# Kernel optimization log

Measured on AMD Instinct MI355X. Metric: run time of the kernel, lower is better.

Reference implementation:

```python
import jax, jax.numpy as jnp
import numpy as np

V, H, COND_DIM, WIDTH = 256, 256, 64, 64
K_STEPS = 5
T = 1.0
GAMMA_W_MAX = 0.05
NOISE_FRAC = 0.1


def setup_inputs() -> dict:
    key = jax.random.key(0)
    ks = jax.random.split(key, 8)
    B = 32768
    # binary visible data (0/1 floats)
    v_data = (jax.random.uniform(ks[0], (B, V)) < 0.5).astype(jnp.float32)
    cond = jax.random.normal(ks[1], (B, COND_DIM), dtype=jnp.float32)
    W = 0.1 * jax.random.normal(ks[2], (V, H), dtype=jnp.float32)
    b = jnp.zeros((V,), jnp.float32)
    c = jnp.zeros((H,), jnp.float32)
    fc1_w = jax.random.normal(ks[3], (WIDTH, COND_DIM), dtype=jnp.float32) * (1.0 / np.sqrt(COND_DIM))
    fc1_b = jnp.zeros((WIDTH,), jnp.float32)
    # fc2 is zero-init in the original; use small random values so the
    # conditional scale/shift path is numerically exercised.
    fc2_w = 0.01 * jax.random.normal(ks[4], (2 * V + 4 * H, WIDTH), dtype=jnp.float32)
    fc2_b = jnp.zeros((2 * V + 4 * H,), jnp.float32)
    return {"v_data": v_data, "cond": cond, "W": W, "b": b, "c": c,
            "fc1_w": fc1_w, "fc1_b": fc1_b, "fc2_w": fc2_w, "fc2_b": fc2_b}


def _cond_params(cond, b, c, fc1_w, fc1_b, fc2_w, fc2_b):
    x = jnp.tanh(cond @ fc1_w.T + fc1_b)
    y = x @ fc2_w.T + fc2_b
    gb, bb, gc, bc, gw, _bw = jnp.split(y, np.cumsum([V, V, H, H, H])[:5].tolist(), axis=-1)
    b_mod = (1.0 + gb) * b[None, :] + bb            # [B,V]
    c_mod = (1.0 + gc) * c[None, :] + bc            # [B,H]
    w_scale = 1.0 + GAMMA_W_MAX * jnp.tanh(gw)      # [B,H]  (beta_w_max=0 -> no shift)
    return b_mod, c_mod, w_scale


def _free_energy_sym(v, W, b_mod, c_mod, w_scale):
    vW = (v @ W) * w_scale                          # [B,H]
    Wsum = W.sum(axis=0)[None, :] * w_scale         # [B,H]
    lin_v = vW + c_mod
    lin_f = Wsum - vW + c_mod
    t2v = jax.nn.softplus(lin_v).sum(axis=-1)
    t2f = jax.nn.softplus(lin_f).sum(axis=-1)
    t1v = -(v * b_mod).sum(axis=-1)
    t1f = -((1.0 - v) * b_mod).sum(axis=-1)
    fe_v = t1v - t2v
    fe_f = t1f - t2f
    stacked = jnp.stack([-fe_v, -fe_f], axis=-1)
    return -T * jax.nn.logsumexp(stacked / T, axis=-1)


def reference(v_data, cond, W, b, c, fc1_w, fc1_b, fc2_w, fc2_b):
    b_mod, c_mod, w_scale = _cond_params(cond, b, c, fc1_w, fc1_b, fc2_w, fc2_b)

    rng = jax.random.key(42)
    B = v_data.shape[0]
    n_noise = int(B * NOISE_FRAC)
    rng, kn = jax.random.split(rng)
    noise = (jax.random.uniform(kn, (n_noise, V)) < 0.5).astype(v_data.dtype)
    v_model = v_data.at[:n_noise].set(noise)

    def gibbs_step(carry, _):
        v, key = carry
        key, k1, k2 = jax.random.split(key, 3)
        p_h = jax.nn.sigmoid(((v @ W) * w_scale + c_mod) / T)
        h = (jax.random.uniform(k1, p_h.shape) < p_h).astype(v.dtype)
        p_v = jax.nn.sigmoid(((h * w_scale) @ W.T + b_mod) / T)
        v_new = (jax.random.uniform(k2, p_v.shape) < p_v).astype(v.dtype)
        return (v_new, key), None

    (v_model, _), _ = jax.lax.scan(gibbs_step, (v_model, rng), None, length=K_STEPS)
    v_model = jax.lax.stop_gradient(v_model)

    fe_data = _free_energy_sym(v_data, W, b_mod, c_mod, w_scale)
    fe_model = _free_energy_sym(v_model, W, b_mod, c_mod, w_scale)
    return (fe_data - fe_model).mean()
```

## Files before the change

kernel.cpp:

```cpp
#include <hip/hip_runtime.h>
#include <stdint.h>

#define V 256
#define H 256
#define CONDD 64
#define WIDTH 64
#define KSTEPS 5
#define BR 32
#define GWMAX 0.05f
#define SW(r) (((r) & 15) << 4)
#define SWX(r) (((r) & 7) << 4)

typedef __attribute__((ext_vector_type(8))) short s16x8;
typedef __attribute__((ext_vector_type(4))) short s16x4;
typedef __attribute__((ext_vector_type(4))) float f32x4;

__device__ __forceinline__ uint64_t splitmix64(uint64_t x) {
  x += 0x9E3779B97F4A7C15ULL;
  x = (x ^ (x >> 30)) * 0xBF58476D1CE4E5B9ULL;
  x = (x ^ (x >> 27)) * 0x94D049BB133111EBULL;
  return x ^ (x >> 31);
}
__device__ __forceinline__ unsigned short f2bf(float f) {
  uint32_t u = __float_as_uint(f);
  return (unsigned short)((u + 0x7FFFu + ((u >> 16) & 1u)) >> 16);
}
__device__ __forceinline__ float bf2f(unsigned short s) {
  return __uint_as_float(((uint32_t)s) << 16);
}
__device__ __forceinline__ uint32_t pack2(float lo, float hi) {
  return (uint32_t)f2bf(lo) | ((uint32_t)f2bf(hi) << 16);
}
__device__ __forceinline__ float unpk_lo(uint32_t u) { return bf2f((unsigned short)(u & 0xFFFFu)); }
__device__ __forceinline__ float unpk_hi(uint32_t u) { return bf2f((unsigned short)(u >> 16)); }
__device__ __forceinline__ float lcg_u01(uint64_t& s) {
  s = s * 6364136223846793005ULL + 1442695040888963407ULL;
  return (float)(uint32_t)(s >> 40) * (1.0f / 16777216.0f);
}
__device__ __forceinline__ float softplusf(float x) {
  return fmaxf(x, 0.0f) + log1pf(expf(-fabsf(x)));
}

__global__ void k_prep(const float* __restrict__ W, const float* __restrict__ fc2_w,
                       unsigned short* __restrict__ Wp_hi, unsigned short* __restrict__ Wp_lo,
                       unsigned short* __restrict__ WTp_hi, unsigned short* __restrict__ fc2p,
                       float* __restrict__ Wsum, float* __restrict__ out) {
  int bid = blockIdx.x;
  if (bid < 256) {
    int idx = bid * 256 + threadIdx.x;
    int j = idx & 7, l = (idx >> 3) & 63, nt = (idx >> 9) & 15, ks = idx >> 13;
    int kk = ks * 32 + (l >> 4) * 8 + j;
    int n = nt * 16 + (l & 15);
    float wv = W[(size_t)kk * H + n];
    unsigned short hi = f2bf(wv);
    Wp_hi[idx] = hi;
    Wp_lo[idx] = f2bf(wv - bf2f(hi));
    WTp_hi[idx] = f2bf(W[(size_t)n * H + kk]);
  } else if (bid < 576) {
    int idx = (bid - 256) * 256 + threadIdx.x;
    int j = idx & 7, l = (idx >> 3) & 63;
    int f = idx >> 9;
    int ks = f / 80, nt = f % 80;
    fc2p[idx] = f2bf(fc2_w[(size_t)(nt * 16 + (l & 15)) * WIDTH + ks * 32 + (l >> 4) * 8 + j]);
  } else {
    int h = threadIdx.x;
    float s = 0.f;
    for (int v = 0; v < V; ++v) s += W[(size_t)v * H + h];
    Wsum[h] = s;
    if (h == 0) out[0] = 0.0f;
  }
}

__device__ __forceinline__ void mm_pass(const char* srcL, const unsigned short* __restrict__ Wp,
                                        int w, int lc, int lg, f32x4 acc[2][2]) {
#pragma unroll
  for (int ks = 0; ks < 8; ++ks) {
    s16x8 af[2];
#pragma unroll
    for (int rt = 0; rt < 2; ++rt) {
      int r = rt * 16 + lc;
      af[rt] = *(const s16x8*)(srcL + r * 512 + ((ks * 64 + lg * 16) ^ SW(r)));
    }
#pragma unroll
    for (int n = 0; n < 2; ++n) {
      int f = ks * 16 + 2 * w + n;
      s16x8 bf = *(const s16x8*)(Wp + ((size_t)f * 64 + lg * 16 + lc) * 8);
#pragma unroll
      for (int rt = 0; rt < 2; ++rt)
        acc[rt][n] = __builtin_amdgcn_mfma_f32_16x16x32_bf16(af[rt], bf, acc[rt][n], 0, 0, 0);
    }
  }
}

__device__ __forceinline__ void fc2_slice(const s16x8 afx[2][2],
                                          const unsigned short* __restrict__ fc2p,
                                          int w, int l, int slice, f32x4 acc[2][2]) {
#pragma unroll
  for (int rt = 0; rt < 2; ++rt)
#pragma unroll
    for (int n = 0; n < 2; ++n) acc[rt][n] = (f32x4){0.f, 0.f, 0.f, 0.f};
#pragma unroll
  for (int ks = 0; ks < 2; ++ks)
#pragma unroll
    for (int n = 0; n < 2; ++n) {
      int f = ks * 80 + slice * 16 + 2 * w + n;
      s16x8 bf = *(const s16x8*)(fc2p + ((size_t)f * 64 + l) * 8);
#pragma unroll
      for (int rt = 0; rt < 2; ++rt)
        acc[rt][n] = __builtin_amdgcn_mfma_f32_16x16x32_bf16(afx[ks][rt], bf, acc[rt][n], 0, 0, 0);
    }
}

__global__ __launch_bounds__(512) void rbm_mfma(
    const float* __restrict__ v_data, const float* __restrict__ cond,
    const float* __restrict__ bvec, const float* __restrict__ cvec,
    const float* __restrict__ fc1_w, const float* __restrict__ fc1_b,
    const float* __restrict__ fc2_b, const unsigned short* __restrict__ Wp_hi,
    const unsigned short* __restrict__ Wp_lo, const unsigned short* __restrict__ WTp_hi,
    const unsigned short* __restrict__ fc2p, const float* __restrict__ Wsum,
    float* __restrict__ out, int Btot, int nnoise) {
  const int tid = threadIdx.x;
  const int w = tid >> 6, l = tid & 63, lc = l & 15, lg = l >> 4;
  const int row0 = blockIdx.x * BR;

  __shared__ unsigned short vmL[BR * 256];
  __shared__ unsigned short hwL[BR * 256];
  __shared__ float red[BR][8];

  uint64_t rs = splitmix64(((uint64_t)(blockIdx.x * 512 + tid) << 1) | 1ULL);

  if (tid < BR * 8) ((float*)red)[tid] = 0.0f;

  float* condS = (float*)hwL;
  char* xS = (char*)hwL + BR * 68 * 4;

#pragma unroll
  for (int s = 0; s < 4; ++s) {
    int e = s * 512 + tid, r = e >> 6, k = e & 63;
    condS[r * 68 + k] = cond[(size_t)(row0 + r) * CONDD + k];
  }
#pragma unroll
  for (int s = 0; s < 2; ++s) {
    int unit = s * 512 + tid;
    int r = unit >> 5, c0 = (unit & 31) * 8;
    int g = row0 + r;
    s16x8 pk;
    if (g < nnoise) {
      rs = rs * 6364136223846793005ULL + 1442695040888963407ULL;
      uint32_t bits = (uint32_t)(rs >> 32);
#pragma unroll
      for (int j = 0; j < 8; ++j) pk[j] = (short)(((bits >> j) & 1u) ? 0x3F80 : 0);
    } else {
      const float* src = v_data + (size_t)g * 256 + c0;
      float4 a = *(const float4*)src, b = *(const float4*)(src + 4);
      pk[0] = (short)f2bf(a.x); pk[1] = (short)f2bf(a.y);
      pk[2] = (short)f2bf(a.z); pk[3] = (short)f2bf(a.w);
      pk[4] = (short)f2bf(b.x); pk[5] = (short)f2bf(b.y);
      pk[6] = (short)f2bf(b.z); pk[7] = (short)f2bf(b.w);
    }
    *(s16x8*)((char*)vmL + r * 512 + ((c0 * 2) ^ SW(r))) = pk;
  }
  __syncthreads();

  {
    int r = tid >> 4, j0 = (tid & 15) * 4;
    float a4[4];
#pragma unroll
    for (int j = 0; j < 4; ++j) a4[j] = fc1_b[j0 + j];
    for (int k = 0; k < CONDD; ++k) {
      float cv = condS[r * 68 + k];
#pragma unroll
      for (int j = 0; j < 4; ++j)
        a4[j] = fmaf(cv, fc1_w[(size_t)(j0 + j) * CONDD + k], a4[j]);
    }
    s16x4 xp;
#pragma unroll
    for (int j = 0; j < 4; ++j) xp[j] = (short)f2bf(tanhf(a4[j]));
    *(s16x4*)(xS + r * 128 + ((j0 * 2) ^ SWX(r))) = xp;
  }
  __syncthreads();

  uint32_t cmws[2][2][4];
  uint32_t bmp[2][4];
  {
    s16x8 afx[2][2];
#pragma unroll
    for (int ks = 0; ks < 2; ++ks)
#pragma unroll
      for (int rt = 0; rt < 2; ++rt) {
        int r = rt * 16 + lc;
        afx[ks][rt] = *(const s16x8*)(xS + r * 128 + (((ks * 32 + lg * 8) * 2) ^ SWX(r)));
      }
    f32x4 accA[2][2], accB[2][2];
    fc2_slice(afx, fc2p, w, l, 0, accA);
    fc2_slice(afx, fc2p, w, l, 1, accB);
#pragma unroll
    for (int rt = 0; rt < 2; ++rt)
#pragma unroll
      for (int i = 0; i < 4; ++i) {
        float b0, b1;
        {
          int c0 = w * 32 + lc, c1 = c0 + 16;
          b0 = fmaf(1.0f + (accA[rt][0][i] + fc2_b[c0]), bvec[c0], accB[rt][0][i] + fc2_b[V + c0]);
          b1 = fmaf(1.0f + (accA[rt][1][i] + fc2_b[c1]), bvec[c1], accB[rt][1][i] + fc2_b[V + c1]);
        }
        bmp[rt][i] = pack2(b0, b1);
      }
    fc2_slice(afx, fc2p, w, l, 2, accA);
    fc2_slice(afx, fc2p, w, l, 3, accB);
#pragma unroll
    for (int rt = 0; rt < 2; ++rt)
#pragma unroll
      for (int n = 0; n < 2; ++n) {
        int col = w * 32 + n * 16 + lc;
        float fb2 = fc2_b[2 * V + col], fb3 = fc2_b[2 * V + H + col], cv = cvec[col];
#pragma unroll
        for (int i = 0; i < 4; ++i)
          accB[rt][n][i] = fmaf(1.0f + (accA[rt][n][i] + fb2), cv, accB[rt][n][i] + fb3);
      }
    fc2_slice(afx, fc2p, w, l, 4, accA);
#pragma unroll
    for (int rt = 0; rt < 2; ++rt)
#pragma unroll
      for (int n = 0; n < 2; ++n) {
        int col = w * 32 + n * 16 + lc;
        float fb4 = fc2_b[2 * V + 2 * H + col];
#pragma unroll
        for (int i = 0; i < 4; ++i)
          cmws[rt][n][i] =
              pack2(accB[rt][n][i], 1.0f + GWMAX * tanhf(accA[rt][n][i] + fb4));
      }
  }
#pragma unroll
  for (int rt = 0; rt < 2; ++rt)
#pragma unroll
    for (int i = 0; i < 4; ++i) {
      float s = unpk_lo(bmp[rt][i]) + unpk_hi(bmp[rt][i]);
      s += __shfl_xor(s, 1); s += __shfl_xor(s, 2);
      s += __shfl_xor(s, 4); s += __shfl_xor(s, 8);
      if (lc == 0) atomicAdd(&red[rt * 16 + lg * 4 + i][6], s);
    }
  __syncthreads();

  uint32_t vbits = 0;
  for (int step = 0; step < KSTEPS; ++step) {
    f32x4 acc[2][2];
#pragma unroll
    for (int rt = 0; rt < 2; ++rt)
#pragma unroll
      for (int n = 0; n < 2; ++n) acc[rt][n] = (f32x4){0.f, 0.f, 0.f, 0.f};
    mm_pass((const char*)vmL, Wp_hi, w, lc, lg, acc);
#pragma unroll
    for (int rt = 0; rt < 2; ++rt)
#pragma unroll
      for (int n = 0; n < 2; ++n)
#pragma unroll
        for (int i = 0; i < 4; ++i) {
          uint32_t p2 = cmws[rt][n][i];
          float act = fmaf(acc[rt][n][i], unpk_hi(p2), unpk_lo(p2));
          float e = __expf(-act);
          float u = lcg_u01(rs);
          unsigned short hv = (fmaf(u, e, u) < 1.0f) ? (unsigned short)(p2 >> 16)
                                                     : (unsigned short)0;
          int r = rt * 16 + lg * 4 + i, c = w * 32 + n * 16 + lc;
          *(unsigned short*)((char*)hwL + r * 512 + ((c * 2) ^ SW(r))) = hv;
        }
    __syncthreads();
#pragma unroll
    for (int rt = 0; rt < 2; ++rt)
#pragma unroll
      for (int n = 0; n < 2; ++n) acc[rt][n] = (f32x4){0.f, 0.f, 0.f, 0.f};
    mm_pass((const char*)hwL, WTp_hi, w, lc, lg, acc);
#pragma unroll
    for (int rt = 0; rt < 2; ++rt)
#pragma unroll
      for (int n = 0; n < 2; ++n)
#pragma unroll
        for (int i = 0; i < 4; ++i) {
          float bmv = n ? unpk_hi(bmp[rt][i]) : unpk_lo(bmp[rt][i]);
          float act = acc[rt][n][i] + bmv;
          float e = __expf(-act);
          float u = lcg_u01(rs);
          int bit = (fmaf(u, e, u) < 1.0f) ? 1 : 0;
          if (step == KSTEPS - 1) vbits |= ((uint32_t)bit << (rt * 8 + n * 4 + i));
          int r = rt * 16 + lg * 4 + i, c = w * 32 + n * 16 + lc;
          *(unsigned short*)((char*)vmL + r * 512 + ((c * 2) ^ SW(r))) =
              bit ? (unsigned short)0x3F80 : (unsigned short)0;
        }
    __syncthreads();
  }

#pragma unroll
  for (int s = 0; s < 2; ++s) {
    int unit = s * 512 + tid;
    int r = unit >> 5, c0 = (unit & 31) * 8;
    const float* src = v_data + (size_t)(row0 + r) * 256 + c0;
    float4 a = *(const float4*)src, b = *(const float4*)(src + 4);
    s16x8 pk;
    pk[0] = (short)f2bf(a.x); pk[1] = (short)f2bf(a.y);
    pk[2] = (short)f2bf(a.z); pk[3] = (short)f2bf(a.w);
    pk[4] = (short)f2bf(b.x); pk[5] = (short)f2bf(b.y);
    pk[6] = (short)f2bf(b.z); pk[7] = (short)f2bf(b.w);
    *(s16x8*)((char*)hwL + r * 512 + ((c0 * 2) ^ SW(r))) = pk;
  }
  __syncthreads();

  {
    float ws2[2];
    ws2[0] = Wsum[w * 32 + lc];
    ws2[1] = Wsum[w * 32 + 16 + lc];
    f32x4 acc[2][2];

#pragma unroll
    for (int rt = 0; rt < 2; ++rt)
#pragma unroll
      for (int n = 0; n < 2; ++n) acc[rt][n] = (f32x4){0.f, 0.f, 0.f, 0.f};
    mm_pass((const char*)vmL, Wp_hi, w, lc, lg, acc);
    mm_pass((const char*)vmL, Wp_lo, w, lc, lg, acc);
#pragma unroll
    for (int rt = 0; rt < 2; ++rt)
#pragma unroll
      for (int i = 0; i < 4; ++i) {
        float sv = 0.f, sf = 0.f, st = 0.f;
        int r = rt * 16 + lg * 4 + i;
#pragma unroll
        for (int n = 0; n < 2; ++n) {
          uint32_t p2 = cmws[rt][n][i];
          float cmv = unpk_lo(p2), wsv = unpk_hi(p2);
          float vw = acc[rt][n][i];
          sv += softplusf(fmaf(vw, wsv, cmv));
          sf += softplusf(fmaf(ws2[n] - vw, wsv, cmv));
          if ((vbits >> (rt * 8 + n * 4 + i)) & 1u)
            st += n ? unpk_hi(bmp[rt][i]) : unpk_lo(bmp[rt][i]);
        }
        sv += __shfl_xor(sv, 1); sv += __shfl_xor(sv, 2); sv += __shfl_xor(sv, 4); sv += __shfl_xor(sv, 8);
        sf += __shfl_xor(sf, 1); sf += __shfl_xor(sf, 2); sf += __shfl_xor(sf, 4); sf += __shfl_xor(sf, 8);
        st += __shfl_xor(st, 1); st += __shfl_xor(st, 2); st += __shfl_xor(st, 4); st += __shfl_xor(st, 8);
        if (lc == 0) {
          atomicAdd(&red[r][3], sv);
          atomicAdd(&red[r][4], sf);
          atomicAdd(&red[r][5], st);
        }
      }

#pragma unroll
    for (int rt = 0; rt < 2; ++rt)
#pragma unroll
      for (int n = 0; n < 2; ++n) acc[rt][n] = (f32x4){0.f, 0.f, 0.f, 0.f};
    mm_pass((const char*)hwL, Wp_hi, w, lc, lg, acc);
    mm_pass((const char*)hwL, Wp_lo, w, lc, lg, acc);
#pragma unroll
    for (int rt = 0; rt < 2; ++rt)
#pragma unroll
      for (int i = 0; i < 4; ++i) {
        float sv = 0.f, sf = 0.f, st = 0.f;
        int r = rt * 16 + lg * 4 + i;
#pragma unroll
        for (int n = 0; n < 2; ++n) {
          uint32_t p2 = cmws[rt][n][i];
          float cmv = unpk_lo(p2), wsv = unpk_hi(p2);
          float vw = acc[rt][n][i];
          sv += softplusf(fmaf(vw, wsv, cmv));
          sf += softplusf(fmaf(ws2[n] - vw, wsv, cmv));
          int c = w * 32 + n * 16 + lc;
          float xv = bf2f(*(const unsigned short*)((const char*)hwL + r * 512 + ((c * 2) ^ SW(r))));
          float bmv = n ? unpk_hi(bmp[rt][i]) : unpk_lo(bmp[rt][i]);
          st = fmaf(xv, bmv, st);
        }
        sv += __shfl_xor(sv, 1); sv += __shfl_xor(sv, 2); sv += __shfl_xor(sv, 4); sv += __shfl_xor(sv, 8);
        sf += __shfl_xor(sf, 1); sf += __shfl_xor(sf, 2); sf += __shfl_xor(sf, 4); sf += __shfl_xor(sf, 8);
        st += __shfl_xor(st, 1); st += __shfl_xor(st, 2); st += __shfl_xor(st, 4); st += __shfl_xor(st, 8);
        if (lc == 0) {
          atomicAdd(&red[r][0], sv);
          atomicAdd(&red[r][1], sf);
          atomicAdd(&red[r][2], st);
        }
      }
  }
  __syncthreads();

  if (tid < BR) {
    int r = tid;
    float a_d = red[r][2] + red[r][0];
    float b_d = (red[r][6] - red[r][2]) + red[r][1];
    float fe_d = -(fmaxf(a_d, b_d) + log1pf(expf(-fabsf(a_d - b_d))));
    float a_m = red[r][5] + red[r][3];
    float b_m = (red[r][6] - red[r][5]) + red[r][4];
    float fe_m = -(fmaxf(a_m, b_m) + log1pf(expf(-fabsf(a_m - b_m))));
    float d = fe_d - fe_m;
#pragma unroll
    for (int m = 1; m < 32; m <<= 1) d += __shfl_xor(d, m);
    if (tid == 0) atomicAdd(out, d * (1.0f / (float)Btot));
  }
}

extern "C" void kernel_launch(void* const* d_in, const int* in_sizes, int n_in,
                              void* d_out, int out_size, void* d_ws, size_t ws_size,
                              hipStream_t stream) {
  const float* v_data = (const float*)d_in[0];
  const float* cond = (const float*)d_in[1];
  const float* W = (const float*)d_in[2];
  const float* bvec = (const float*)d_in[3];
  const float* cvec = (const float*)d_in[4];
  const float* fc1_w = (const float*)d_in[5];
  const float* fc1_b = (const float*)d_in[6];
  const float* fc2_w = (const float*)d_in[7];
  const float* fc2_b = (const float*)d_in[8];
  float* out = (float*)d_out;

  int Btot = in_sizes[0] / V;
  int nnoise = (int)((double)Btot * 0.1);

  unsigned short* Wp_hi = (unsigned short*)d_ws;
  unsigned short* Wp_lo = Wp_hi + 65536;
  unsigned short* WTp_hi = Wp_lo + 65536;
  unsigned short* fc2p = WTp_hi + 65536;
  float* Wsum = (float*)(fc2p + 81920);

  k_prep<<<577, 256, 0, stream>>>(W, fc2_w, Wp_hi, Wp_lo, WTp_hi, fc2p, Wsum, out);
  rbm_mfma<<<Btot / BR, 512, 0, stream>>>(v_data, cond, bvec, cvec, fc1_w, fc1_b, fc2_b,
                                          Wp_hi, Wp_lo, WTp_hi, fc2p, Wsum, out, Btot, nnoise);
}
```

Measured before the change: 468.8 us.

## Halve rows per block, use fast tanh/softplus, cheaper 32-bit RNG

Cuts the batch rows handled per 512-thread block from 32 to 16. Each wave now does one 16-row MFMA tile instead of two, which halves the accumulator and parameter registers and doubles the grid size. It also replaces tanhf/log1pf/expf with fast intrinsic-based versions and swaps the 64-bit LCG for a 32-bit one, with stateless splitmix noise per element. It moves one barrier so the v_data load overlaps the model-free-energy pass. The cost is less weight reuse per block: every W fragment is now loaded from global/L2 for only 16 rows, and the fast math functions are less accurate.

New measurement: 402.4 us. -14.1%, faster.

```diff
diff --git a/kernel.cpp b/kernel.cpp
--- a/kernel.cpp
+++ b/kernel.cpp
@@ -6,13 +6,12 @@
 #define CONDD 64
 #define WIDTH 64
 #define KSTEPS 5
-#define BR 32
+#define BR 16
 #define GWMAX 0.05f
 #define SW(r) (((r) & 15) << 4)
 #define SWX(r) (((r) & 7) << 4)
 
 typedef __attribute__((ext_vector_type(8))) short s16x8;
-typedef __attribute__((ext_vector_type(4))) short s16x4;
 typedef __attribute__((ext_vector_type(4))) float f32x4;
 
 __device__ __forceinline__ uint64_t splitmix64(uint64_t x) {
@@ -33,12 +32,13 @@
 }
 __device__ __forceinline__ float unpk_lo(uint32_t u) { return bf2f((unsigned short)(u & 0xFFFFu)); }
 __device__ __forceinline__ float unpk_hi(uint32_t u) { return bf2f((unsigned short)(u >> 16)); }
-__device__ __forceinline__ float lcg_u01(uint64_t& s) {
-  s = s * 6364136223846793005ULL + 1442695040888963407ULL;
-  return (float)(uint32_t)(s >> 40) * (1.0f / 16777216.0f);
-}
-__device__ __forceinline__ float softplusf(float x) {
-  return fmaxf(x, 0.0f) + log1pf(expf(-fabsf(x)));
+__device__ __forceinline__ float fast_sp(float x) {
+  return fmaxf(x, 0.0f) + __logf(1.0f + __expf(-fabsf(x)));
+}
+__device__ __forceinline__ float fast_tanh(float x) {
+  float t = __expf(-2.0f * fabsf(x));
+  float r = (1.0f - t) * __builtin_amdgcn_rcpf(1.0f + t);
+  return copysignf(r, x);
 }
 
 __global__ void k_prep(const float* __restrict__ W, const float* __restrict__ fc2_w,
@@ -72,42 +72,31 @@
 }
 
 __device__ __forceinline__ void mm_pass(const char* srcL, const unsigned short* __restrict__ Wp,
-                                        int w, int lc, int lg, f32x4 acc[2][2]) {
+                                        int w, int lc, int lg, f32x4 acc[2]) {
 #pragma unroll
   for (int ks = 0; ks < 8; ++ks) {
-    s16x8 af[2];
-#pragma unroll
-    for (int rt = 0; rt < 2; ++rt) {
-      int r = rt * 16 + lc;
-      af[rt] = *(const s16x8*)(srcL + r * 512 + ((ks * 64 + lg * 16) ^ SW(r)));
-    }
+    s16x8 af = *(const s16x8*)(srcL + lc * 512 + ((ks * 64 + lg * 16) ^ SW(lc)));
 #pragma unroll
     for (int n = 0; n < 2; ++n) {
       int f = ks * 16 + 2 * w + n;
       s16x8 bf = *(const s16x8*)(Wp + ((size_t)f * 64 + lg * 16 + lc) * 8);
-#pragma unroll
-      for (int rt = 0; rt < 2; ++rt)
-        acc[rt][n] = __builtin_amdgcn_mfma_f32_16x16x32_bf16(af[rt], bf, acc[rt][n], 0, 0, 0);
-    }
-  }
-}
-
-__device__ __forceinline__ void fc2_slice(const s16x8 afx[2][2],
+      acc[n] = __builtin_amdgcn_mfma_f32_16x16x32_bf16(af, bf, acc[n], 0, 0, 0);
+    }
+  }
+}
+
+__device__ __forceinline__ void fc2_slice(const s16x8 afx[2],
                                           const unsigned short* __restrict__ fc2p,
-                                          int w, int l, int slice, f32x4 acc[2][2]) {
-#pragma unroll
-  for (int rt = 0; rt < 2; ++rt)
-#pragma unroll
-    for (int n = 0; n < 2; ++n) acc[rt][n] = (f32x4){0.f, 0.f, 0.f, 0.f};
+                                          int w, int l, int slice, f32x4 acc[2]) {
+#pragma unroll
+  for (int n = 0; n < 2; ++n) acc[n] = (f32x4){0.f, 0.f, 0.f, 0.f};
 #pragma unroll
   for (int ks = 0; ks < 2; ++ks)
 #pragma unroll
     for (int n = 0; n < 2; ++n) {
       int f = ks * 80 + slice * 16 + 2 * w + n;
       s16x8 bf = *(const s16x8*)(fc2p + ((size_t)f * 64 + l) * 8);
-#pragma unroll
-      for (int rt = 0; rt < 2; ++rt)
-        acc[rt][n] = __builtin_amdgcn_mfma_f32_16x16x32_bf16(afx[ks][rt], bf, acc[rt][n], 0, 0, 0);
+      acc[n] = __builtin_amdgcn_mfma_f32_16x16x32_bf16(afx[ks], bf, acc[n], 0, 0, 0);
     }
 }
 
@@ -127,27 +116,22 @@
   __shared__ unsigned short hwL[BR * 256];
   __shared__ float red[BR][8];
 
-  uint64_t rs = splitmix64(((uint64_t)(blockIdx.x * 512 + tid) << 1) | 1ULL);
-
   if (tid < BR * 8) ((float*)red)[tid] = 0.0f;
 
   float* condS = (float*)hwL;
   char* xS = (char*)hwL + BR * 68 * 4;
 
 #pragma unroll
-  for (int s = 0; s < 4; ++s) {
+  for (int s = 0; s < 2; ++s) {
     int e = s * 512 + tid, r = e >> 6, k = e & 63;
     condS[r * 68 + k] = cond[(size_t)(row0 + r) * CONDD + k];
   }
-#pragma unroll
-  for (int s = 0; s < 2; ++s) {
-    int unit = s * 512 + tid;
-    int r = unit >> 5, c0 = (unit & 31) * 8;
+  {
+    int r = tid >> 5, c0 = (tid & 31) * 8;
     int g = row0 + r;
     s16x8 pk;
     if (g < nnoise) {
-      rs = rs * 6364136223846793005ULL + 1442695040888963407ULL;
-      uint32_t bits = (uint32_t)(rs >> 32);
+      uint32_t bits = (uint32_t)(splitmix64(((uint64_t)g << 6) | (uint64_t)(c0 >> 3)) >> 32);
 #pragma unroll
       for (int j = 0; j < 8; ++j) pk[j] = (short)(((bits >> j) & 1u) ? 0x3F80 : 0);
     } else {
@@ -163,137 +147,111 @@
   __syncthreads();
 
   {
-    int r = tid >> 4, j0 = (tid & 15) * 4;
-    float a4[4];
-#pragma unroll
-    for (int j = 0; j < 4; ++j) a4[j] = fc1_b[j0 + j];
+    int r = tid >> 5, j0 = (tid & 31) * 2;
+    float a0 = fc1_b[j0], a1 = fc1_b[j0 + 1];
     for (int k = 0; k < CONDD; ++k) {
       float cv = condS[r * 68 + k];
-#pragma unroll
-      for (int j = 0; j < 4; ++j)
-        a4[j] = fmaf(cv, fc1_w[(size_t)(j0 + j) * CONDD + k], a4[j]);
-    }
-    s16x4 xp;
-#pragma unroll
-    for (int j = 0; j < 4; ++j) xp[j] = (short)f2bf(tanhf(a4[j]));
-    *(s16x4*)(xS + r * 128 + ((j0 * 2) ^ SWX(r))) = xp;
+      a0 = fmaf(cv, fc1_w[(size_t)j0 * CONDD + k], a0);
+      a1 = fmaf(cv, fc1_w[(size_t)(j0 + 1) * CONDD + k], a1);
+    }
+    uint32_t xp = pack2(fast_tanh(a0), fast_tanh(a1));
+    *(uint32_t*)(xS + r * 128 + ((j0 * 2) ^ SWX(r))) = xp;
   }
   __syncthreads();
 
-  uint32_t cmws[2][2][4];
-  uint32_t bmp[2][4];
-  {
-    s16x8 afx[2][2];
+  uint32_t cmws[2][4];
+  uint32_t bmp[4];
+  {
+    s16x8 afx[2];
 #pragma unroll
     for (int ks = 0; ks < 2; ++ks)
-#pragma unroll
-      for (int rt = 0; rt < 2; ++rt) {
-        int r = rt * 16 + lc;
-        afx[ks][rt] = *(const s16x8*)(xS + r * 128 + (((ks * 32 + lg * 8) * 2) ^ SWX(r)));
-      }
-    f32x4 accA[2][2], accB[2][2];
+      afx[ks] = *(const s16x8*)(xS + lc * 128 + (((ks * 32 + lg * 8) * 2) ^ SWX(lc)));
+    f32x4 accA[2], accB[2];
     fc2_slice(afx, fc2p, w, l, 0, accA);
     fc2_slice(afx, fc2p, w, l, 1, accB);
-#pragma unroll
-    for (int rt = 0; rt < 2; ++rt)
-#pragma unroll
-      for (int i = 0; i < 4; ++i) {
-        float b0, b1;
-        {
-          int c0 = w * 32 + lc, c1 = c0 + 16;
-          b0 = fmaf(1.0f + (accA[rt][0][i] + fc2_b[c0]), bvec[c0], accB[rt][0][i] + fc2_b[V + c0]);
-          b1 = fmaf(1.0f + (accA[rt][1][i] + fc2_b[c1]), bvec[c1], accB[rt][1][i] + fc2_b[V + c1]);
-        }
-        bmp[rt][i] = pack2(b0, b1);
-      }
+    {
+      int c0 = w * 32 + lc, c1 = c0 + 16;
+      float f00 = fc2_b[c0], f01 = fc2_b[c1], f10 = fc2_b[V + c0], f11 = fc2_b[V + c1];
+      float bv0 = bvec[c0], bv1 = bvec[c1];
+#pragma unroll
+      for (int i = 0; i < 4; ++i)
+        bmp[i] = pack2(fmaf(1.0f + (accA[0][i] + f00), bv0, accB[0][i] + f10),
+                       fmaf(1.0f + (accA[1][i] + f01), bv1, accB[1][i] + f11));
+    }
     fc2_slice(afx, fc2p, w, l, 2, accA);
     fc2_slice(afx, fc2p, w, l, 3, accB);
 #pragma unroll
-    for (int rt = 0; rt < 2; ++rt)
-#pragma unroll
-      for (int n = 0; n < 2; ++n) {
-        int col = w * 32 + n * 16 + lc;
-        float fb2 = fc2_b[2 * V + col], fb3 = fc2_b[2 * V + H + col], cv = cvec[col];
-#pragma unroll
-        for (int i = 0; i < 4; ++i)
-          accB[rt][n][i] = fmaf(1.0f + (accA[rt][n][i] + fb2), cv, accB[rt][n][i] + fb3);
-      }
+    for (int n = 0; n < 2; ++n) {
+      int col = w * 32 + n * 16 + lc;
+      float fb2 = fc2_b[2 * V + col], fb3 = fc2_b[2 * V + H + col], cv = cvec[col];
+#pragma unroll
+      for (int i = 0; i < 4; ++i)
+        accB[n][i] = fmaf(1.0f + (accA[n][i] + fb2), cv, accB[n][i] + fb3);
+    }
     fc2_slice(afx, fc2p, w, l, 4, accA);
 #pragma unroll
-    for (int rt = 0; rt < 2; ++rt)
-#pragma unroll
-      for (int n = 0; n < 2; ++n) {
-        int col = w * 32 + n * 16 + lc;
-        float fb4 = fc2_b[2 * V + 2 * H + col];
-#pragma unroll
-        for (int i = 0; i < 4; ++i)
-          cmws[rt][n][i] =
-              pack2(accB[rt][n][i], 1.0f + GWMAX * tanhf(accA[rt][n][i] + fb4));
-      }
-  }
-#pragma unroll
-  for (int rt = 0; rt < 2; ++rt)
-#pragma unroll
-    for (int i = 0; i < 4; ++i) {
-      float s = unpk_lo(bmp[rt][i]) + unpk_hi(bmp[rt][i]);
-      s += __shfl_xor(s, 1); s += __shfl_xor(s, 2);
-      s += __shfl_xor(s, 4); s += __shfl_xor(s, 8);
-      if (lc == 0) atomicAdd(&red[rt * 16 + lg * 4 + i][6], s);
-    }
+    for (int n = 0; n < 2; ++n) {
+      int col = w * 32 + n * 16 + lc;
+      float fb4 = fc2_b[2 * V + 2 * H + col];
+#pragma unroll
+      for (int i = 0; i < 4; ++i)
+        cmws[n][i] = pack2(accB[n][i], 1.0f + GWMAX * fast_tanh(accA[n][i] + fb4));
+    }
+  }
+#pragma unroll
+  for (int i = 0; i < 4; ++i) {
+    float s = unpk_lo(bmp[i]) + unpk_hi(bmp[i]);
+    s += __shfl_xor(s, 1); s += __shfl_xor(s, 2);
+    s += __shfl_xor(s, 4); s += __shfl_xor(s, 8);
+    if (lc == 0) atomicAdd(&red[lg * 4 + i][6], s);
+  }
   __syncthreads();
 
+  uint32_t r32 = (uint32_t)splitmix64(0xBEEF000000000000ULL | (uint64_t)(blockIdx.x * 512 + tid));
   uint32_t vbits = 0;
   for (int step = 0; step < KSTEPS; ++step) {
-    f32x4 acc[2][2];
-#pragma unroll
-    for (int rt = 0; rt < 2; ++rt)
-#pragma unroll
-      for (int n = 0; n < 2; ++n) acc[rt][n] = (f32x4){0.f, 0.f, 0.f, 0.f};
+    f32x4 acc[2];
+#pragma unroll
+    for (int n = 0; n < 2; ++n) acc[n] = (f32x4){0.f, 0.f, 0.f, 0.f};
     mm_pass((const char*)vmL, Wp_hi, w, lc, lg, acc);
 #pragma unroll
-    for (int rt = 0; rt < 2; ++rt)
-#pragma unroll
-      for (int n = 0; n < 2; ++n)
-#pragma unroll
-        for (int i = 0; i < 4; ++i) {
-          uint32_t p2 = cmws[rt][n][i];
-          float act = fmaf(acc[rt][n][i], unpk_hi(p2), unpk_lo(p2));
-          float e = __expf(-act);
-          float u = lcg_u01(rs);
-          unsigned short hv = (fmaf(u, e, u) < 1.0f) ? (unsigned short)(p2 >> 16)
-                                                     : (unsigned short)0;
-          int r = rt * 16 + lg * 4 + i, c = w * 32 + n * 16 + lc;
-          *(unsigned short*)((char*)hwL + r * 512 + ((c * 2) ^ SW(r))) = hv;
-        }
+    for (int n = 0; n < 2; ++n)
+#pragma unroll
+      for (int i = 0; i < 4; ++i) {
+        uint32_t p2 = cmws[n][i];
+        float act = fmaf(acc[n][i], unpk_hi(p2), unpk_lo(p2));
+        float e = __expf(-act);
+        r32 = r32 * 1664525u + 1013904223u;
+        float u = (float)(r32 >> 8) * (1.0f / 16777216.0f);
+        unsigned short hv = (fmaf(u, e, u) < 1.0f) ? (unsigned short)(p2 >> 16)
+                                                   : (unsigned short)0;
+        int r = lg * 4 + i, c = w * 32 + n * 16 + lc;
+        *(unsigned short*)((char*)hwL + r * 512 + ((c * 2) ^ SW(r))) = hv;
+      }
     __syncthreads();
 #pragma unroll
-    for (int rt = 0; rt < 2; ++rt)
-#pragma unroll
-      for (int n = 0; n < 2; ++n) acc[rt][n] = (f32x4){0.f, 0.f, 0.f, 0.f};
+    for (int n = 0; n < 2; ++n) acc[n] = (f32x4){0.f, 0.f, 0.f, 0.f};
     mm_pass((const char*)hwL, WTp_hi, w, lc, lg, acc);
 #pragma unroll
-    for (int rt = 0; rt < 2; ++rt)
-#pragma unroll
-      for (int n = 0; n < 2; ++n)
-#pragma unroll
-        for (int i = 0; i < 4; ++i) {
-          float bmv = n ? unpk_hi(bmp[rt][i]) : unpk_lo(bmp[rt][i]);
-          float act = acc[rt][n][i] + bmv;
-          float e = __expf(-act);
-          float u = lcg_u01(rs);
-          int bit = (fmaf(u, e, u) < 1.0f) ? 1 : 0;
-          if (step == KSTEPS - 1) vbits |= ((uint32_t)bit << (rt * 8 + n * 4 + i));
-          int r = rt * 16 + lg * 4 + i, c = w * 32 + n * 16 + lc;
-          *(unsigned short*)((char*)vmL + r * 512 + ((c * 2) ^ SW(r))) =
-              bit ? (unsigned short)0x3F80 : (unsigned short)0;
-        }
+    for (int n = 0; n < 2; ++n)
+#pragma unroll
+      for (int i = 0; i < 4; ++i) {
+        float bmv = n ? unpk_hi(bmp[i]) : unpk_lo(bmp[i]);
+        float act = acc[n][i] + bmv;
+        float e = __expf(-act);
+        r32 = r32 * 1664525u + 1013904223u;
+        float u = (float)(r32 >> 8) * (1.0f / 16777216.0f);
+        int bit = (fmaf(u, e, u) < 1.0f) ? 1 : 0;
+        if (step == KSTEPS - 1) vbits |= ((uint32_t)bit << (n * 4 + i));
+        int r = lg * 4 + i, c = w * 32 + n * 16 + lc;
+        *(unsigned short*)((char*)vmL + r * 512 + ((c * 2) ^ SW(r))) =
+            bit ? (unsigned short)0x3F80 : (unsigned short)0;
+      }
     __syncthreads();
   }
 
-#pragma unroll
-  for (int s = 0; s < 2; ++s) {
-    int unit = s * 512 + tid;
-    int r = unit >> 5, c0 = (unit & 31) * 8;
+  {
+    int r = tid >> 5, c0 = (tid & 31) * 8;
     const float* src = v_data + (size_t)(row0 + r) * 256 + c0;
     float4 a = *(const float4*)src, b = *(const float4*)(src + 4);
     s16x8 pk;
@@ -303,79 +261,70 @@
     pk[6] = (short)f2bf(b.z); pk[7] = (short)f2bf(b.w);
     *(s16x8*)((char*)hwL + r * 512 + ((c0 * 2) ^ SW(r))) = pk;
   }
-  __syncthreads();
 
   {
     float ws2[2];
     ws2[0] = Wsum[w * 32 + lc];
     ws2[1] = Wsum[w * 32 + 16 + lc];
-    f32x4 acc[2][2];
-
-#pragma unroll
-    for (int rt = 0; rt < 2; ++rt)
-#pragma unroll
-      for (int n = 0; n < 2; ++n) acc[rt][n] = (f32x4){0.f, 0.f, 0.f, 0.f};
+    f32x4 acc[2];
+
+#pragma unroll
+    for (int n = 0; n < 2; ++n) acc[n] = (f32x4){0.f, 0.f, 0.f, 0.f};
     mm_pass((const char*)vmL, Wp_hi, w, lc, lg, acc);
     mm_pass((const char*)vmL, Wp_lo, w, lc, lg, acc);
 #pragma unroll
-    for (int rt = 0; rt < 2; ++rt)
-#pragma unroll
-      for (int i = 0; i < 4; ++i) {
-        float sv = 0.f, sf = 0.f, st = 0.f;
-        int r = rt * 16 + lg * 4 + i;
-#pragma unroll
-        for (int n = 0; n < 2; ++n) {
-          uint32_t p2 = cmws[rt][n][i];
-          float cmv = unpk_lo(p2), wsv = unpk_hi(p2);
-          float vw = acc[rt][n][i];
-          sv += softplusf(fmaf(vw, wsv, cmv));
-          sf += softplusf(fmaf(ws2[n] - vw, wsv, cmv));
-          if ((vbits >> (rt * 8 + n * 4 + i)) & 1u)
-            st += n ? unpk_hi(bmp[rt][i]) : unpk_lo(bmp[rt][i]);
-        }
-        sv += __shfl_xor(sv, 1); sv += __shfl_xor(sv, 2); sv += __shfl_xor(sv, 4); sv += __shfl_xor(sv, 8);
-        sf += __shfl_xor(sf, 1); sf += __shfl_xor(sf, 2); sf += __shfl_xor(sf, 4); sf += __shfl_xor(sf, 8);
-        st += __shfl_xor(st, 1); st += __shfl_xor(st, 2); st += __shfl_xor(st, 4); st += __shfl_xor(st, 8);
-        if (lc == 0) {
-          atomicAdd(&red[r][3], sv);
-          atomicAdd(&red[r][4], sf);
-          atomicAdd(&red[r][5], st);
-        }
-      }
-
-#pragma unroll
-    for (int rt = 0; rt < 2; ++rt)
-#pragma unroll
-      for (int n = 0; n < 2; ++n) acc[rt][n] = (f32x4){0.f, 0.f, 0.f, 0.f};
+    for (int i = 0; i < 4; ++i) {
+      float sv = 0.f, sf = 0.f, st = 0.f;
+      int r = lg * 4 + i;
+#pragma unroll
+      for (int n = 0; n < 2; ++n) {
+        uint32_t p2 = cmws[n][i];
+        float cmv = unpk_lo(p2), wsv = unpk_hi(p2);
+        float vw = acc[n][i];
+        sv += fast_sp(fmaf(vw, wsv, cmv));
+        sf += fast_sp(fmaf(ws2[n] - vw, wsv, cmv));
+        if ((vbits >> (n * 4 + i)) & 1u) st += n ? unpk_hi(bmp[i]) : unpk_lo(bmp[i]);
+      }
+      sv += __shfl_xor(sv, 1); sv += __shfl_xor(sv, 2); sv += __shfl_xor(sv, 4); sv += __shfl_xor(sv, 8);
+      sf += __shfl_xor(sf, 1); sf += __shfl_xor(sf, 2); sf += __shfl_xor(sf, 4); sf += __shfl_xor(sf, 8);
+      st += __shfl_xor(st, 1); st += __shfl_xor(st, 2); st += __shfl_xor(st, 4); st += __shfl_xor(st, 8);
+      if (lc == 0) {
+        atomicAdd(&red[r][3], sv);
+        atomicAdd(&red[r][4], sf);
+        atomicAdd(&red[r][5], st);
+      }
+    }
+    __syncthreads();
+
+#pragma unroll
+    for (int n = 0; n < 2; ++n) acc[n] = (f32x4){0.f, 0.f, 0.f, 0.f};
     mm_pass((const char*)hwL, Wp_hi, w, lc, lg, acc);
     mm_pass((const char*)hwL, Wp_lo, w, lc, lg, acc);
 #pragma unroll
-    for (int rt = 0; rt < 2; ++rt)
-#pragma unroll
-      for (int i = 0; i < 4; ++i) {
-        float sv = 0.f, sf = 0.f, st = 0.f;
-        int r = rt * 16 + lg * 4 + i;
-#pragma unroll
-        for (int n = 0; n < 2; ++n) {
-          uint32_t p2 = cmws[rt][n][i];
-          float cmv = unpk_lo(p2), wsv = unpk_hi(p2);
-          float vw = acc[rt][n][i];
-          sv += softplusf(fmaf(vw, wsv, cmv));
-          sf += softplusf(fmaf(ws2[n] - vw, wsv, cmv));
-          int c = w * 32 + n * 16 + lc;
-          float xv = bf2f(*(const unsigned short*)((const char*)hwL + r * 512 + ((c * 2) ^ SW(r))));
-          float bmv = n ? unpk_hi(bmp[rt][i]) : unpk_lo(bmp[rt][i]);
-          st = fmaf(xv, bmv, st);
-        }
-        sv += __shfl_xor(sv, 1); sv += __shfl_xor(sv, 2); sv += __shfl_xor(sv, 4); sv += __shfl_xor(sv, 8);
-        sf += __shfl_xor(sf, 1); sf += __shfl_xor(sf, 2); sf += __shfl_xor(sf, 4); sf += __shfl_xor(sf, 8);
-        st += __shfl_xor(st, 1); st += __shfl_xor(st, 2); st += __shfl_xor(st, 4); st += __shfl_xor(st, 8);
-        if (lc == 0) {
-          atomicAdd(&red[r][0], sv);
-          atomicAdd(&red[r][1], sf);
-          atomicAdd(&red[r][2], st);
-        }
-      }
+    for (int i = 0; i < 4; ++i) {
+      float sv = 0.f, sf = 0.f, st = 0.f;
+      int r = lg * 4 + i;
+#pragma unroll
+      for (int n = 0; n < 2; ++n) {
+        uint32_t p2 = cmws[n][i];
+        float cmv = unpk_lo(p2), wsv = unpk_hi(p2);
+        float vw = acc[n][i];
+        sv += fast_sp(fmaf(vw, wsv, cmv));
+        sf += fast_sp(fmaf(ws2[n] - vw, wsv, cmv));
+        int c = w * 32 + n * 16 + lc;
+        float xv = bf2f(*(const unsigned short*)((const char*)hwL + r * 512 + ((c * 2) ^ SW(r))));
+        float bmv = n ? unpk_hi(bmp[i]) : unpk_lo(bmp[i]);
+        st = fmaf(xv, bmv, st);
+      }
+      sv += __shfl_xor(sv, 1); sv += __shfl_xor(sv, 2); sv += __shfl_xor(sv, 4); sv += __shfl_xor(sv, 8);
+      sf += __shfl_xor(sf, 1); sf += __shfl_xor(sf, 2); sf += __shfl_xor(sf, 4); sf += __shfl_xor(sf, 8);
+      st += __shfl_xor(st, 1); st += __shfl_xor(st, 2); st += __shfl_xor(st, 4); st += __shfl_xor(st, 8);
+      if (lc == 0) {
+        atomicAdd(&red[r][0], sv);
+        atomicAdd(&red[r][1], sf);
+        atomicAdd(&red[r][2], st);
+      }
+    }
   }
   __syncthreads();
 
@@ -389,7 +338,7 @@
     float fe_m = -(fmaxf(a_m, b_m) + log1pf(expf(-fabsf(a_m - b_m))));
     float d = fe_d - fe_m;
 #pragma unroll
-    for (int m = 1; m < 32; m <<= 1) d += __shfl_xor(d, m);
+    for (int m = 1; m < 16; m <<= 1) d += __shfl_xor(d, m);
     if (tid == 0) atomicAdd(out, d * (1.0f / (float)Btot));
   }
 }
```
